# Performance work log

Hardware: AMD Instinct MI355X
Metric: run time of the kernel (lower is better)

## Reference

```python
import jax, jax.numpy as jnp
from jax import lax
import numpy as np

NUM_TAGS = 64
BATCH = 512
SEQ_LEN = 512


def setup_inputs() -> dict:
    key = jax.random.key(0)
    k1, k2, k3, k4 = jax.random.split(key, 4)
    emissions = jax.random.normal(k1, (BATCH, SEQ_LEN, NUM_TAGS), dtype=jnp.float32)
    tags = jax.random.randint(k2, (BATCH, SEQ_LEN), 0, NUM_TAGS, dtype=jnp.int32).astype(jnp.int64)
    # variable-length sequences: lengths in [SEQ_LEN//2, SEQ_LEN]
    lengths = jax.random.randint(k3, (BATCH,), SEQ_LEN // 2, SEQ_LEN + 1)
    mask = (jnp.arange(SEQ_LEN)[None, :] < lengths[:, None]).astype(jnp.float32)
    # transitions parameter (num_tags+2, num_tags+2) with START/STOP constraints
    start_idx, stop_idx = NUM_TAGS, NUM_TAGS + 1
    t = jax.random.uniform(k4, (NUM_TAGS + 2, NUM_TAGS + 2), minval=-0.1, maxval=0.1, dtype=jnp.float32)
    t = t.at[start_idx, :].set(-100.0)  # no transitions TO start
    t = t.at[:, stop_idx].set(-100.0)   # no transitions FROM stop
    return {"emissions": emissions, "tags": tags, "mask": mask, "transitions": t}


def reference(emissions, tags, mask, transitions):
    B, S, T = emissions.shape
    start_idx, stop_idx = T, T + 1
    mask = mask.astype(emissions.dtype)
    tags = tags.astype(jnp.int32)
    bidx = jnp.arange(B)

    # ---- gold path score (vectorized over time) ----
    first = tags[:, 0]
    gold = (emissions[bidx, 0, first] + transitions[first, start_idx]) * mask[:, 0]
    curr = tags[:, 1:]                       # (B, S-1)
    prev = tags[:, :-1]                      # (B, S-1)
    trans_sc = transitions[curr, prev]       # (B, S-1)
    emit_sc = jnp.take_along_axis(emissions[:, 1:], curr[:, :, None], axis=2)[:, :, 0]
    gold = gold + jnp.sum((trans_sc + emit_sc) * mask[:, 1:], axis=1)
    lengths = jnp.sum(mask, axis=1).astype(jnp.int32)
    last = tags[bidx, lengths - 1]
    gold = gold + transitions[stop_idx, last]

    # ---- partition function via sequential logsumexp scan ----
    tt = transitions[:T, :T]                 # (T_prev -> row is curr? matches torch indexing [curr, prev])
    score0 = (emissions[:, 0] + transitions[:T, start_idx][None, :]) * mask[:, 0, None]

    def step(score, xs):
        emit, m = xs                         # (B, T), (B,)
        # torch: prev_score (B,T,1) + transitions (T,T) -> logsumexp over dim 1 (prev tags)
        ns = jax.nn.logsumexp(score[:, :, None] + tt[None, :, :], axis=1)
        return ns + emit * m[:, None], None

    emits = jnp.swapaxes(emissions[:, 1:], 0, 1)  # (S-1, B, T)
    ms = mask[:, 1:].T                            # (S-1, B)
    score_f, _ = lax.scan(step, score0, (emits, ms))
    score_f = score_f + transitions[stop_idx, :T][None, :]
    logZ = jax.nn.logsumexp(score_f, axis=1)

    return jnp.mean(logZ - gold)
```

## Files before the change

### kernel.cpp

```cpp
#include <hip/hip_runtime.h>

#define BB 512
#define SS 512
#define TT 64
#define TSTRIDE 66
#define MID 256

typedef _Float16 h2 __attribute__((ext_vector_type(2)));

static __device__ __forceinline__ float first_lane(float v) {
    return __int_as_float(__builtin_amdgcn_readfirstlane(__float_as_int(v)));
}
static __device__ __forceinline__ unsigned pk_f16(float a, float b) {
    return __builtin_bit_cast(unsigned, __builtin_amdgcn_cvt_pkrtz(a, b));
}
static __device__ __forceinline__ h2 as_h2(unsigned u) {
    return __builtin_bit_cast(h2, u);
}
#define FDOT2(a, b, c) __builtin_amdgcn_fdot2((a), (b), (c), false)

#define DO32(F) F(0) F(1) F(2) F(3) F(4) F(5) F(6) F(7) \
                F(8) F(9) F(10) F(11) F(12) F(13) F(14) F(15) \
                F(16) F(17) F(18) F(19) F(20) F(21) F(22) F(23) \
                F(24) F(25) F(26) F(27) F(28) F(29) F(30) F(31)

__global__ __launch_bounds__(64)
__attribute__((amdgpu_waves_per_eu(1, 1)))
void crf_scan2_kernel(
    const float* __restrict__ emissions,
    const float* __restrict__ mask,
    const float* __restrict__ trans,
    float* __restrict__ ws_state)
{
    __shared__ unsigned EQ[32][64];
    __shared__ uint4 PLv[8];

    const int blk = blockIdx.x;
    const int b   = blk >> 1;
    const int dir = blk & 1;
    const int j   = threadIdx.x;

    const float* em = emissions + (size_t)b * SS * TT;
    const float* mk = mask + (size_t)b * SS;
    unsigned short* PL = (unsigned short*)PLv;
    const uint4* PV = (const uint4*)PLv;

    if (dir == 0) {
        #pragma unroll
        for (int w = 0; w < 32; ++w)
            EQ[w][j] = pk_f16(__expf(trans[(2 * w) * TSTRIDE + j]),
                              __expf(trans[(2 * w + 1) * TSTRIDE + j]));
    } else {
        #pragma unroll
        for (int w = 0; w < 32; ++w)
            EQ[w][j] = pk_f16(__expf(trans[j * TSTRIDE + 2 * w]),
                              __expf(trans[j * TSTRIDE + 2 * w + 1]));
    }
    __syncthreads();

#define CDECL(K) const unsigned c##K = EQ[K][j];
    DO32(CDECL)
#undef CDECL

#define DOT4(D, CA, CB, CC, CD) \
    a0_ = FDOT2(as_h2((D).x), as_h2(CA), a0_); \
    a1_ = FDOT2(as_h2((D).y), as_h2(CB), a1_); \
    a2_ = FDOT2(as_h2((D).z), as_h2(CC), a2_); \
    a3_ = FDOT2(as_h2((D).w), as_h2(CD), a3_);

#define STEPC(PRE, POST, CADD) do { \
        float m0c = first_lane(sc) + (CADD); \
        float p   = __expf(sc + (PRE) - m0c); \
        PL[j] = (unsigned short)(pk_f16(p, p) & 0xFFFF); \
        uint4 d0 = PV[0], d1 = PV[1], d2 = PV[2], d3 = PV[3]; \
        uint4 d4 = PV[4], d5 = PV[5], d6 = PV[6], d7 = PV[7]; \
        float a0_ = 0.f, a1_ = 0.f, a2_ = 0.f, a3_ = 0.f; \
        DOT4(d0, c0,  c1,  c2,  c3)  DOT4(d1, c4,  c5,  c6,  c7) \
        DOT4(d2, c8,  c9,  c10, c11) DOT4(d3, c12, c13, c14, c15) \
        DOT4(d4, c16, c17, c18, c19) DOT4(d5, c20, c21, c22, c23) \
        DOT4(d6, c24, c25, c26, c27) DOT4(d7, c28, c29, c30, c31) \
        sc = m0c + __logf((a0_ + a1_) + (a2_ + a3_)) + (POST); \
    } while (0)

    float sc;
    if (dir == 0) {
        sc = em[j] + trans[j * TSTRIDE + TT];
        float r0 = em[1 * TT + j], r1 = em[2 * TT + j];
        float r2 = em[3 * TT + j], r3 = em[4 * TT + j];
        float r4 = em[5 * TT + j], r5 = em[6 * TT + j];
        float r6 = em[7 * TT + j], r7 = em[8 * TT + j];
        const float* pe = em + 9 * TT + j;
        for (int it = 0; it < 31; ++it) {
            float n0 = pe[0],   n1 = pe[64],  n2 = pe[128], n3 = pe[192];
            float n4 = pe[256], n5 = pe[320], n6 = pe[384], n7 = pe[448];
            pe += 512;
            STEPC(0.0f, r0, 4.0f); STEPC(0.0f, r1, 4.0f);
            STEPC(0.0f, r2, 4.0f); STEPC(0.0f, r3, 4.0f);
            STEPC(0.0f, r4, 4.0f); STEPC(0.0f, r5, 4.0f);
            STEPC(0.0f, r6, 4.0f); STEPC(0.0f, r7, 4.0f);
            r0 = n0; r1 = n1; r2 = n2; r3 = n3;
            r4 = n4; r5 = n5; r6 = n6; r7 = n7;
        }
        STEPC(0.0f, r0, 4.0f); STEPC(0.0f, r1, 4.0f);
        STEPC(0.0f, r2, 4.0f); STEPC(0.0f, r3, 4.0f);
        STEPC(0.0f, r4, 4.0f); STEPC(0.0f, r5, 4.0f);
        STEPC(0.0f, r6, 4.0f);
        ws_state[(size_t)b * 128 + j] = sc;
    } else {
        float msum = 0.f;
        #pragma unroll
        for (int t = 0; t < 8; ++t) msum += mk[j + 64 * t];
        #pragma unroll
        for (int off = 32; off; off >>= 1) msum += __shfl_xor(msum, off);
        const int len = (int)(first_lane(msum) + 0.5f);

        sc = trans[65 * TSTRIDE + j];
        float r0 = em[511 * TT + j], r1 = em[510 * TT + j];
        float r2 = em[509 * TT + j], r3 = em[508 * TT + j];
        float r4 = em[507 * TT + j], r5 = em[506 * TT + j];
        float r6 = em[505 * TT + j], r7 = em[504 * TT + j];
        const float* pe = em + 503 * TT + j;
        int scur = 511;
#define BEE(RK, SV) (((SV) < len) ? (RK) : 0.0f)
        for (int it = 0; it < 31; ++it) {
            float n0 = pe[0],    n1 = pe[-64],  n2 = pe[-128], n3 = pe[-192];
            float n4 = pe[-256], n5 = pe[-320], n6 = pe[-384], n7 = pe[-448];
            pe -= 512;
            STEPC(BEE(r0, scur - 0), 0.0f, 5.0f);
            STEPC(BEE(r1, scur - 1), 0.0f, 5.0f);
            STEPC(BEE(r2, scur - 2), 0.0f, 5.0f);
            STEPC(BEE(r3, scur - 3), 0.0f, 5.0f);
            STEPC(BEE(r4, scur - 4), 0.0f, 5.0f);
            STEPC(BEE(r5, scur - 5), 0.0f, 5.0f);
            STEPC(BEE(r6, scur - 6), 0.0f, 5.0f);
            STEPC(BEE(r7, scur - 7), 0.0f, 5.0f);
            scur -= 8;
            r0 = n0; r1 = n1; r2 = n2; r3 = n3;
            r4 = n4; r5 = n5; r6 = n6; r7 = n7;
        }
        STEPC(BEE(r0, 263), 0.0f, 5.0f); STEPC(BEE(r1, 262), 0.0f, 5.0f);
        STEPC(BEE(r2, 261), 0.0f, 5.0f); STEPC(BEE(r3, 260), 0.0f, 5.0f);
        STEPC(BEE(r4, 259), 0.0f, 5.0f); STEPC(BEE(r5, 258), 0.0f, 5.0f);
        STEPC(BEE(r6, 257), 0.0f, 5.0f); STEPC(BEE(r7, 256), 0.0f, 5.0f);
#undef BEE
        ws_state[(size_t)b * 128 + 64 + j] = sc;
    }
#undef STEPC
#undef DOT4
}

__global__ __launch_bounds__(64) void crf_combine_kernel(
    const float* __restrict__ emissions,
    const int*   __restrict__ tags,
    const float* __restrict__ mask,
    const float* __restrict__ trans,
    const float* __restrict__ ws_state,
    float* __restrict__ diff_out)
{
    const int b = blockIdx.x;
    const int j = threadIdx.x;
    const float* em = emissions + (size_t)b * SS * TT;
    const float* mk = mask + (size_t)b * SS;

    float v = ws_state[(size_t)b * 128 + j] + ws_state[(size_t)b * 128 + 64 + j];
    float m = v;
    #pragma unroll
    for (int off = 32; off; off >>= 1) m = fmaxf(m, __shfl_xor(m, off));
    float e = __expf(v - m);
    #pragma unroll
    for (int off = 32; off; off >>= 1) e += __shfl_xor(e, off);
    float zres = m + __logf(e);

    float msum = 0.f;
    #pragma unroll
    for (int t = 0; t < 8; ++t) msum += mk[j + 64 * t];
    #pragma unroll
    for (int off = 32; off; off >>= 1) msum += __shfl_xor(msum, off);
    const int len = (int)(first_lane(msum) + 0.5f);

    const int* tg = tags + (size_t)b * SS;
    float acc = 0.f;
    for (int s = j; s < SS; s += 64) {
        if (s < len) {
            if (s > 0) {
                int curr = tg[s], prev = tg[s - 1];
                acc += trans[curr * TSTRIDE + prev] + em[s * TT + curr];
            } else {
                int t0_ = tg[0];
                acc += em[t0_] + trans[t0_ * TSTRIDE + TT];
            }
        }
    }
    #pragma unroll
    for (int off = 32; off; off >>= 1) acc += __shfl_xor(acc, off);
    if (j == 0) {
        int last = tg[len - 1];
        acc += trans[65 * TSTRIDE + last];
        diff_out[b] = zres - acc;
    }
}

__global__ __launch_bounds__(256) void crf_final_kernel(
    const float* __restrict__ diff,
    float* __restrict__ out)
{
    __shared__ float sdata[4];
    int t = threadIdx.x;
    float v = 0.f;
    for (int i = t; i < BB; i += 256) v += diff[i];
    #pragma unroll
    for (int off = 32; off; off >>= 1) v += __shfl_xor(v, off);
    if ((t & 63) == 0) sdata[t >> 6] = v;
    __syncthreads();
    if (t == 0) out[0] = (sdata[0] + sdata[1] + sdata[2] + sdata[3]) * (1.0f / BB);
}

extern "C" void kernel_launch(void* const* d_in, const int* in_sizes, int n_in,
                              void* d_out, int out_size, void* d_ws, size_t ws_size,
                              hipStream_t stream) {
    const float* emissions = (const float*)d_in[0];
    const int*   tags      = (const int*)d_in[1];
    const float* mask      = (const float*)d_in[2];
    const float* trans     = (const float*)d_in[3];
    float* out  = (float*)d_out;
    float* ws_state = (float*)d_ws;
    float* diff = ws_state + (size_t)BB * 128;

    crf_scan2_kernel<<<2 * BB, 64, 0, stream>>>(emissions, mask, trans, ws_state);
    crf_combine_kernel<<<BB, 64, 0, stream>>>(emissions, tags, mask, trans,
                                              ws_state, diff);
    crf_final_kernel<<<1, 256, 0, stream>>>(diff, out);
}
```

Before: 64.21 us.

## Replace LDS broadcast of scan probabilities with DPP/swizzle/permlane cross-lane exchange

Each scan step used to write per-lane half-precision probabilities to shared memory and read all 64 back as eight uint4 loads. It now assembles the needed packed pairs in registers with DPP moves, ds_swizzle and permlane32_swap (falling back to bpermute), and permutes the transition matrix layout so each lane's constants match the lane-exchange pattern. This targets the LDS store/load round trip and its wait latency on the serial dependency chain. The cost is more cross-lane instructions per step, plus some correctness risk in the permutation mapping.

```diff
diff --git a/kernel.cpp b/kernel.cpp
--- a/kernel.cpp
+++ b/kernel.cpp
@@ -4,9 +4,9 @@
 #define SS 512
 #define TT 64
 #define TSTRIDE 66
-#define MID 256
 
 typedef _Float16 h2 __attribute__((ext_vector_type(2)));
+typedef int i2v __attribute__((ext_vector_type(2)));
 
 static __device__ __forceinline__ float first_lane(float v) {
     return __int_as_float(__builtin_amdgcn_readfirstlane(__float_as_int(v)));
@@ -17,7 +17,13 @@
 static __device__ __forceinline__ h2 as_h2(unsigned u) {
     return __builtin_bit_cast(h2, u);
 }
+static __device__ __forceinline__ unsigned bperm(int addr, unsigned v) {
+    return (unsigned)__builtin_amdgcn_ds_bpermute(addr, (int)v);
+}
 #define FDOT2(a, b, c) __builtin_amdgcn_fdot2((a), (b), (c), false)
+#define DPPF(v, ctrl) __int_as_float(__builtin_amdgcn_mov_dpp(__float_as_int(v), (ctrl), 0xF, 0xF, true))
+#define DPPU(v, ctrl) ((unsigned)__builtin_amdgcn_mov_dpp((int)(v), (ctrl), 0xF, 0xF, true))
+#define SWZ16(v) ((unsigned)__builtin_amdgcn_ds_swizzle((int)(v), 0x401F))
 
 #define DO32(F) F(0) F(1) F(2) F(3) F(4) F(5) F(6) F(7) \
                 F(8) F(9) F(10) F(11) F(12) F(13) F(14) F(15) \
@@ -33,28 +39,31 @@
     float* __restrict__ ws_state)
 {
     __shared__ unsigned EQ[32][64];
-    __shared__ uint4 PLv[8];
 
     const int blk = blockIdx.x;
     const int b   = blk >> 1;
     const int dir = blk & 1;
     const int j   = threadIdx.x;
+    const bool lo32 = (j < 32);
+    const int a32v = ((j ^ 32) << 2);
 
     const float* em = emissions + (size_t)b * SS * TT;
     const float* mk = mask + (size_t)b * SS;
-    unsigned short* PL = (unsigned short*)PLv;
-    const uint4* PV = (const uint4*)PLv;
-
-    if (dir == 0) {
+
+    {
+        const int tl[8] = {0, 2, 7, 5, 15, 13, 8, 10};
         #pragma unroll
-        for (int w = 0; w < 32; ++w)
-            EQ[w][j] = pk_f16(__expf(trans[(2 * w) * TSTRIDE + j]),
-                              __expf(trans[(2 * w + 1) * TSTRIDE + j]));
-    } else {
-        #pragma unroll
-        for (int w = 0; w < 32; ++w)
-            EQ[w][j] = pk_f16(__expf(trans[j * TSTRIDE + 2 * w]),
-                              __expf(trans[j * TSTRIDE + 2 * w + 1]));
+        for (int w = 0; w < 32; ++w) {
+            int g = w >> 3, k = w & 7;
+            int i0 = j ^ (g << 4) ^ tl[k];
+            int i1 = i0 ^ 1;
+            if (dir == 0)
+                EQ[w][j] = pk_f16(__expf(trans[i0 * TSTRIDE + j]),
+                                  __expf(trans[i1 * TSTRIDE + j]));
+            else
+                EQ[w][j] = pk_f16(__expf(trans[j * TSTRIDE + i0]),
+                                  __expf(trans[j * TSTRIDE + i1]));
+        }
     }
     __syncthreads();
 
@@ -62,23 +71,66 @@
     DO32(CDECL)
 #undef CDECL
 
-#define DOT4(D, CA, CB, CC, CD) \
-    a0_ = FDOT2(as_h2((D).x), as_h2(CA), a0_); \
-    a1_ = FDOT2(as_h2((D).y), as_h2(CB), a1_); \
-    a2_ = FDOT2(as_h2((D).z), as_h2(CC), a2_); \
-    a3_ = FDOT2(as_h2((D).w), as_h2(CD), a3_);
+#if defined(__has_builtin) && __has_builtin(__builtin_amdgcn_permlane32_swap)
+#define XCH32(DST, SRC) { i2v r_ = __builtin_amdgcn_permlane32_swap((int)(SRC), (int)(SRC), false, false); \
+                          DST = (unsigned)(lo32 ? r_.y : r_.x); }
+#else
+#define XCH32(DST, SRC) { DST = bperm(a32v, (SRC)); }
+#endif
 
 #define STEPC(PRE, POST, CADD) do { \
         float m0c = first_lane(sc) + (CADD); \
         float p   = __expf(sc + (PRE) - m0c); \
-        PL[j] = (unsigned short)(pk_f16(p, p) & 0xFFFF); \
-        uint4 d0 = PV[0], d1 = PV[1], d2 = PV[2], d3 = PV[3]; \
-        uint4 d4 = PV[4], d5 = PV[5], d6 = PV[6], d7 = PV[7]; \
+        float pn_ = DPPF(p, 0xB1); \
+        unsigned W0 = pk_f16(p, pn_); \
+        unsigned W1 = DPPU(W0, 0x4E); \
+        unsigned W2 = DPPU(W0, 0x141); \
+        unsigned W3 = DPPU(W1, 0x141); \
+        unsigned W4 = DPPU(W0, 0x140); \
+        unsigned W5 = DPPU(W1, 0x140); \
+        unsigned W6 = DPPU(W4, 0x141); \
+        unsigned W7 = DPPU(W5, 0x141); \
+        unsigned X0 = SWZ16(W0), X1 = SWZ16(W1), X2 = SWZ16(W2), X3 = SWZ16(W3); \
+        unsigned X4 = SWZ16(W4), X5 = SWZ16(W5), X6 = SWZ16(W6), X7 = SWZ16(W7); \
+        unsigned Y0, Y1, Y2, Y3, Y4, Y5, Y6, Y7; \
+        XCH32(Y0, W0) XCH32(Y1, W1) XCH32(Y2, W2) XCH32(Y3, W3) \
+        XCH32(Y4, W4) XCH32(Y5, W5) XCH32(Y6, W6) XCH32(Y7, W7) \
         float a0_ = 0.f, a1_ = 0.f, a2_ = 0.f, a3_ = 0.f; \
-        DOT4(d0, c0,  c1,  c2,  c3)  DOT4(d1, c4,  c5,  c6,  c7) \
-        DOT4(d2, c8,  c9,  c10, c11) DOT4(d3, c12, c13, c14, c15) \
-        DOT4(d4, c16, c17, c18, c19) DOT4(d5, c20, c21, c22, c23) \
-        DOT4(d6, c24, c25, c26, c27) DOT4(d7, c28, c29, c30, c31) \
+        a0_ = FDOT2(as_h2(W0), as_h2(c0), a0_); \
+        a1_ = FDOT2(as_h2(W1), as_h2(c1), a1_); \
+        a2_ = FDOT2(as_h2(W2), as_h2(c2), a2_); \
+        a3_ = FDOT2(as_h2(W3), as_h2(c3), a3_); \
+        a0_ = FDOT2(as_h2(W4), as_h2(c4), a0_); \
+        a1_ = FDOT2(as_h2(W5), as_h2(c5), a1_); \
+        a2_ = FDOT2(as_h2(W6), as_h2(c6), a2_); \
+        a3_ = FDOT2(as_h2(W7), as_h2(c7), a3_); \
+        a0_ = FDOT2(as_h2(Y0), as_h2(c16), a0_); \
+        a1_ = FDOT2(as_h2(Y1), as_h2(c17), a1_); \
+        a2_ = FDOT2(as_h2(Y2), as_h2(c18), a2_); \
+        a3_ = FDOT2(as_h2(Y3), as_h2(c19), a3_); \
+        a0_ = FDOT2(as_h2(Y4), as_h2(c20), a0_); \
+        a1_ = FDOT2(as_h2(Y5), as_h2(c21), a1_); \
+        a2_ = FDOT2(as_h2(Y6), as_h2(c22), a2_); \
+        a3_ = FDOT2(as_h2(Y7), as_h2(c23), a3_); \
+        unsigned Z0, Z1, Z2, Z3, Z4, Z5, Z6, Z7; \
+        XCH32(Z0, X0) XCH32(Z1, X1) XCH32(Z2, X2) XCH32(Z3, X3) \
+        XCH32(Z4, X4) XCH32(Z5, X5) XCH32(Z6, X6) XCH32(Z7, X7) \
+        a0_ = FDOT2(as_h2(X0), as_h2(c8),  a0_); \
+        a1_ = FDOT2(as_h2(X1), as_h2(c9),  a1_); \
+        a2_ = FDOT2(as_h2(X2), as_h2(c10), a2_); \
+        a3_ = FDOT2(as_h2(X3), as_h2(c11), a3_); \
+        a0_ = FDOT2(as_h2(X4), as_h2(c12), a0_); \
+        a1_ = FDOT2(as_h2(X5), as_h2(c13), a1_); \
+        a2_ = FDOT2(as_h2(X6), as_h2(c14), a2_); \
+        a3_ = FDOT2(as_h2(X7), as_h2(c15), a3_); \
+        a0_ = FDOT2(as_h2(Z0), as_h2(c24), a0_); \
+        a1_ = FDOT2(as_h2(Z1), as_h2(c25), a1_); \
+        a2_ = FDOT2(as_h2(Z2), as_h2(c26), a2_); \
+        a3_ = FDOT2(as_h2(Z3), as_h2(c27), a3_); \
+        a0_ = FDOT2(as_h2(Z4), as_h2(c28), a0_); \
+        a1_ = FDOT2(as_h2(Z5), as_h2(c29), a1_); \
+        a2_ = FDOT2(as_h2(Z6), as_h2(c30), a2_); \
+        a3_ = FDOT2(as_h2(Z7), as_h2(c31), a3_); \
         sc = m0c + __logf((a0_ + a1_) + (a2_ + a3_)) + (POST); \
     } while (0)
 
@@ -146,7 +198,7 @@
         ws_state[(size_t)b * 128 + 64 + j] = sc;
     }
 #undef STEPC
-#undef DOT4
+#undef XCH32
 }
 
 __global__ __launch_bounds__(64) void crf_combine_kernel(
```

Result: slower. 120.2 us (+87.2%).
